# Kernel tuning notes

Hardware: AMD Instinct MI355X
Metric: run time of the kernel (lower is better)

The kernel has to match this reference:

```python
import jax, jax.numpy as jnp
import numpy as np

EPS = 1e-8
M_MARGIN = 0.5  # circle-loss margin m


def _l2norm(x):
    # torch.cosine_similarity clamps the norm product at eps; clamping each norm is equivalent in effect for randn data
    return x / jnp.maximum(jnp.linalg.norm(x, axis=-1, keepdims=True), EPS)


def setup_inputs() -> dict:
    key = jax.random.key(0)
    k1, k2, k3, k4 = jax.random.split(key, 4)
    N, D = 8192, 1024
    return {
        "text_embeddings": jax.random.normal(k1, (N, D), dtype=jnp.float32),
        "text_pos_embeddings": jax.random.normal(k2, (N, D), dtype=jnp.float32),
        "text_neg_embeddings": jax.random.normal(k3, (N, D), dtype=jnp.float32),
        "text_neg_index": jax.random.randint(k4, (N,), 0, N, dtype=jnp.int64 if jax.config.jax_enable_x64 else jnp.int32),
    }


def reference(text_embeddings, text_pos_embeddings, text_neg_embeddings, text_neg_index):
    # use_all_pair=False, mixcse=-1 branch of RetriContrastLoss.forward
    q = _l2norm(text_embeddings)        # [N, D]
    p = _l2norm(text_pos_embeddings)    # [N, D]
    n = _l2norm(text_neg_embeddings)    # [M, D]

    # normalize-then-GEMM == cosine_similarity(unsqueeze(1), unsqueeze(0))
    sim_neg = jnp.einsum("nd,md->nm", q, n)       # [N, M] query-vs-neg cosines
    sim_pos = jnp.sum(q * p, axis=-1)             # [N]    query-vs-pos diagonal cosines
    # NOTE: temperature is never applied in this branch (faithful to source)

    m = M_MARGIN
    # negatives: an = clamp_min(detach(s) + (1+m), 0); s' = an * (s - delta_n), delta_n = -(1-m)
    an = jnp.maximum(jax.lax.stop_gradient(sim_neg) + (1.0 + m), 0.0)
    s_neg = an * (sim_neg + (1.0 - m))
    # positives: ap = clamp_min(-detach(s) + (1+m), 0); s' = -ap * (s - delta_p), delta_p = 1-m
    ap = jnp.maximum(-jax.lax.stop_gradient(sim_pos) + (1.0 + m), 0.0)
    s_pos = -ap * (sim_pos - (1.0 - m))

    # source flattens via boolean mask then logsumexp over dim=0 -> global logsumexp
    lse_neg = jax.scipy.special.logsumexp(s_neg.reshape(-1))
    lse_pos = jax.scipy.special.logsumexp(s_pos)
    return jax.nn.softplus(lse_neg + lse_pos)
```

## Files before the change

### kernel.cpp

```cpp
#include <hip/hip_runtime.h>
#include <hip/hip_bf16.h>
#include <hip/hip_fp8.h>

#define D_K 1024
#define TILE 128
#define ROWB 512
#define KB_ITER 128

typedef int intx8 __attribute__((ext_vector_type(8)));
typedef float floatx4 __attribute__((ext_vector_type(4)));

__device__ __forceinline__ unsigned int f2fp4(float v) {
    const float a = fabsf(v);
    unsigned int c = (unsigned int)(a >= 0.25f) + (a >= 0.75f) + (a >= 1.25f)
                   + (a >= 1.75f) + (a >= 2.5f) + (a >= 3.5f) + (a >= 5.0f);
    return c | (v < 0.0f ? 8u : 0u);
}

__device__ __forceinline__ void gl_lds16(const void* g, void* l) {
    __builtin_amdgcn_global_load_lds(
        (const __attribute__((address_space(1))) unsigned int*)g,
        (__attribute__((address_space(3))) unsigned int*)l,
        16, 0, 0);
}

__device__ __forceinline__ intx8 ld_frag4(const unsigned char* rowbase, int c, int e) {
    const int4 d = *(const int4*)(rowbase + ((c ^ e) * 16));
    intx8 v;
    v[0] = d.x; v[1] = d.y; v[2] = d.z; v[3] = d.w;
    v[4] = 0; v[5] = 0; v[6] = 0; v[7] = 0;
    return v;
}

__global__ __launch_bounds__(256)
void prep_kernel(const float* __restrict__ q, const float* __restrict__ p,
                 const float* __restrict__ ng,
                 unsigned short* __restrict__ qn, unsigned short* __restrict__ nn,
                 float* __restrict__ posp) {
    const int wid = threadIdx.x >> 6, lane = threadIdx.x & 63;
    const int row = blockIdx.x * 4 + wid;
    const size_t base = (size_t)row * D_K;
    const float4* q4 = (const float4*)(q + base);
    const float4* p4 = (const float4*)(p + base);
    const float4* n4 = (const float4*)(ng + base);

    float4 qa[4], na[4];
    float qq = 0.f, pp = 0.f, qp = 0.f, nn2 = 0.f;
#pragma unroll
    for (int j = 0; j < 4; j++) {
        qa[j] = q4[j * 64 + lane];
        float4 pa = p4[j * 64 + lane];
        na[j] = n4[j * 64 + lane];
        qq += qa[j].x*qa[j].x + qa[j].y*qa[j].y + qa[j].z*qa[j].z + qa[j].w*qa[j].w;
        pp += pa.x*pa.x + pa.y*pa.y + pa.z*pa.z + pa.w*pa.w;
        qp += qa[j].x*pa.x + qa[j].y*pa.y + qa[j].z*pa.z + qa[j].w*pa.w;
        nn2 += na[j].x*na[j].x + na[j].y*na[j].y + na[j].z*na[j].z + na[j].w*na[j].w;
    }
#pragma unroll
    for (int off = 1; off < 64; off <<= 1) {
        qq += __shfl_xor(qq, off);
        pp += __shfl_xor(pp, off);
        qp += __shfl_xor(qp, off);
        nn2 += __shfl_xor(nn2, off);
    }
    const float rq = 32.0f / fmaxf(sqrtf(qq), 1e-8f);
    const float rn = 32.0f / fmaxf(sqrtf(nn2), 1e-8f);

    unsigned short* qr = qn + (size_t)row * 256;
    unsigned short* nr = nn + (size_t)row * 256;
#pragma unroll
    for (int j = 0; j < 4; j++) {
        unsigned int w = f2fp4(qa[j].x * rq) | (f2fp4(qa[j].y * rq) << 4)
                       | (f2fp4(qa[j].z * rq) << 8) | (f2fp4(qa[j].w * rq) << 12);
        qr[j * 64 + lane] = (unsigned short)w;
        w = f2fp4(na[j].x * rn) | (f2fp4(na[j].y * rn) << 4)
          | (f2fp4(na[j].z * rn) << 8) | (f2fp4(na[j].w * rn) << 12);
        nr[j * 64 + lane] = (unsigned short)w;
    }

    if (lane == 0) {
        const float rp = 1.0f / fmaxf(sqrtf(pp), 1e-8f);
        const float sim = qp * (rq / 32.0f) * rp;
        const float ap = fmaxf(1.5f - sim, 0.0f);
        const float sp = -ap * (sim - 0.5f);
        posp[row] = __expf(sp - 4.0f);
    }
}

__global__ __launch_bounds__(256, 2)
void gemm_lse_fp4(const unsigned char* __restrict__ A,
                  const unsigned char* __restrict__ B,
                  float* __restrict__ negp) {
    __shared__ unsigned char As[TILE * KB_ITER];
    __shared__ unsigned char Bs[TILE * KB_ITER];

    const int tid = threadIdx.x;
    const int wid = tid >> 6;
    const int lane = tid & 63;
    const int tile_m = blockIdx.y * TILE;
    const int tile_n = blockIdx.x * TILE;

    const int wave_m = (wid & 1) * 64;
    const int wave_n = (wid >> 1) * 64;
    const int quad = lane >> 4;
    const int r = lane & 15;
    const int e = r & 7;

    floatx4 acc[4][4] = {};

    int lds_off[4];
    size_t src_off[4];
#pragma unroll
    for (int s = 0; s < 4; s++) {
        const int cc = s * 256 + tid;
        const int row = cc >> 3, slot = cc & 7;
        lds_off[s] = cc * 16;
        src_off[s] = (size_t)row * ROWB + (size_t)((slot ^ (row & 7)) * 16);
    }
    const unsigned char* Ab = A + (size_t)tile_m * ROWB;
    const unsigned char* Bb = B + (size_t)tile_n * ROWB;

    for (int k0b = 0; k0b < ROWB; k0b += KB_ITER) {
#pragma unroll
        for (int s = 0; s < 4; s++) {
            gl_lds16(Ab + src_off[s] + k0b, &As[lds_off[s]]);
            gl_lds16(Bb + src_off[s] + k0b, &Bs[lds_off[s]]);
        }
        __syncthreads();

#pragma unroll
        for (int t = 0; t < 2; t++) {
            intx8 a[4], b[4];
#pragma unroll
            for (int i = 0; i < 4; i++)
                a[i] = ld_frag4(&As[(wave_m + i * 16 + r) * KB_ITER], t * 4 + quad, e);
#pragma unroll
            for (int j = 0; j < 4; j++)
                b[j] = ld_frag4(&Bs[(wave_n + j * 16 + r) * KB_ITER], t * 4 + quad, e);

#pragma unroll
            for (int i = 0; i < 4; i++)
#pragma unroll
                for (int j = 0; j < 4; j++)
                    acc[i][j] = __builtin_amdgcn_mfma_scale_f32_16x16x128_f8f6f4(
                        a[i], b[j], acc[i][j],
                        4, 4,
                        0, 0x7A7A7A7A,
                        0, 0x7A7A7A7A);
        }

        __syncthreads();
    }

    float lsum = 0.0f;
#pragma unroll
    for (int i = 0; i < 4; i++)
#pragma unroll
        for (int j = 0; j < 4; j++)
#pragma unroll
            for (int el = 0; el < 4; el++) {
                const float s = acc[i][j][el];
                const float an = fmaxf(s + 1.5f, 0.0f);
                const float sn = an * (s + 0.5f);
                lsum += __expf(sn - 4.0f);
            }
    for (int off = 32; off > 0; off >>= 1) lsum += __shfl_down(lsum, off);
    __shared__ float red[4];
    if (lane == 0) red[wid] = lsum;
    __syncthreads();
    if (tid == 0)
        negp[blockIdx.y * gridDim.x + blockIdx.x] = red[0] + red[1] + red[2] + red[3];
}

__global__ __launch_bounds__(1024)
void finalize_kernel(const float* __restrict__ negp, int n_neg,
                     const float* __restrict__ posp, int n_pos,
                     float* __restrict__ out) {
    double sn = 0.0, sp = 0.0;
    for (int i = threadIdx.x; i < n_neg; i += 1024) sn += (double)negp[i];
    for (int i = threadIdx.x; i < n_pos; i += 1024) sp += (double)posp[i];
    for (int off = 32; off > 0; off >>= 1) {
        sn += __shfl_down(sn, off);
        sp += __shfl_down(sp, off);
    }
    __shared__ double rn[16], rp[16];
    const int wid = threadIdx.x >> 6, lane = threadIdx.x & 63;
    if (lane == 0) { rn[wid] = sn; rp[wid] = sp; }
    __syncthreads();
    if (threadIdx.x == 0) {
        double NS = 0.0, PS = 0.0;
#pragma unroll
        for (int w = 0; w < 16; w++) { NS += rn[w]; PS += rp[w]; }
        const double x = (4.0 + log(NS)) + (4.0 + log(PS));
        const double spl = (x > 30.0) ? x : log1p(exp(x));
        out[0] = (float)spl;
    }
}

extern "C" void kernel_launch(void* const* d_in, const int* in_sizes, int n_in,
                              void* d_out, int out_size, void* d_ws, size_t ws_size,
                              hipStream_t stream) {
    const float* q = (const float*)d_in[0];
    const float* p = (const float*)d_in[1];
    const float* ng = (const float*)d_in[2];

    const int N = in_sizes[3];
    const int D = in_sizes[0] / N;
    const int M = in_sizes[2] / D;

    char* ws = (char*)d_ws;
    unsigned short* qn = (unsigned short*)ws;
    unsigned short* nn = (unsigned short*)(ws + (size_t)N * ROWB);
    float* negp = (float*)(ws + (size_t)(N + M) * ROWB);
    const int n_neg = (M / TILE) * (N / TILE);
    float* posp = negp + n_neg;

    prep_kernel<<<N / 4, 256, 0, stream>>>(q, p, ng, qn, nn, posp);
    gemm_lse_fp4<<<dim3(M / TILE, N / TILE), 256, 0, stream>>>(
        (const unsigned char*)qn, (const unsigned char*)nn, negp);
    finalize_kernel<<<1, 1024, 0, stream>>>(negp, n_neg, posp, N, (float*)d_out);
}
```

Measured before the change: 169.5 us.

## Switch FP4 GEMM to 32x32x64 MFMA with larger K stage

Replaces the 16x16x128 scaled MFMA tiling (4x4 fragments per wave) with 32x32x64 scaled MFMAs (2x2 fragments per wave) and doubles the K chunk staged in LDS per iteration to 256 bytes, with a new XOR swizzle. This halves the number of outer loop barriers and fragment loads per MFMA, aiming to reduce LDS traffic and sync overhead. LDS usage doubles (64KB per block), which may limit occupancy to one block per CU despite the launch bound of 2.

New measurement: 174.3 us. 2.9% more time.

```diff
diff --git a/kernel.cpp b/kernel.cpp
--- a/kernel.cpp
+++ b/kernel.cpp
@@ -5,10 +5,10 @@
 #define D_K 1024
 #define TILE 128
 #define ROWB 512
-#define KB_ITER 128
+#define KB_ITER 256
 
 typedef int intx8 __attribute__((ext_vector_type(8)));
-typedef float floatx4 __attribute__((ext_vector_type(4)));
+typedef float floatx16 __attribute__((ext_vector_type(16)));
 
 __device__ __forceinline__ unsigned int f2fp4(float v) {
     const float a = fabsf(v);
@@ -24,12 +24,8 @@
         16, 0, 0);
 }
 
-__device__ __forceinline__ intx8 ld_frag4(const unsigned char* rowbase, int c, int e) {
-    const int4 d = *(const int4*)(rowbase + ((c ^ e) * 16));
-    intx8 v;
-    v[0] = d.x; v[1] = d.y; v[2] = d.z; v[3] = d.w;
-    v[4] = 0; v[5] = 0; v[6] = 0; v[7] = 0;
-    return v;
+__device__ __forceinline__ void ld_lo(intx8* dst, const unsigned char* p) {
+    *(int4*)dst = *(const int4*)p;
 }
 
 __global__ __launch_bounds__(256)
@@ -102,47 +98,49 @@
 
     const int wave_m = (wid & 1) * 64;
     const int wave_n = (wid >> 1) * 64;
-    const int quad = lane >> 4;
-    const int r = lane & 15;
-    const int e = r & 7;
-
-    floatx4 acc[4][4] = {};
-
-    int lds_off[4];
-    size_t src_off[4];
-#pragma unroll
-    for (int s = 0; s < 4; s++) {
-        const int cc = s * 256 + tid;
-        const int row = cc >> 3, slot = cc & 7;
-        lds_off[s] = cc * 16;
-        src_off[s] = (size_t)row * ROWB + (size_t)((slot ^ (row & 7)) * 16);
-    }
+    const int r32 = lane & 31;
+    const int h = lane >> 5;
+    const int e = lane & 7;
+
+    floatx16 acc[2][2] = {};
+
+    intx8 a[2], b[2];
+#pragma unroll
+    for (int i = 0; i < 2; i++) { a[i] = (intx8)0; b[i] = (intx8)0; }
+
     const unsigned char* Ab = A + (size_t)tile_m * ROWB;
     const unsigned char* Bb = B + (size_t)tile_n * ROWB;
 
-    for (int k0b = 0; k0b < ROWB; k0b += KB_ITER) {
-#pragma unroll
-        for (int s = 0; s < 4; s++) {
-            gl_lds16(Ab + src_off[s] + k0b, &As[lds_off[s]]);
-            gl_lds16(Bb + src_off[s] + k0b, &Bs[lds_off[s]]);
+    const unsigned char* arow0 = &As[(wave_m + r32) * KB_ITER];
+    const unsigned char* arow1 = &As[(wave_m + 32 + r32) * KB_ITER];
+    const unsigned char* brow0 = &Bs[(wave_n + r32) * KB_ITER];
+    const unsigned char* brow1 = &Bs[(wave_n + 32 + r32) * KB_ITER];
+
+    for (int kb = 0; kb < ROWB; kb += KB_ITER) {
+#pragma unroll
+        for (int s = 0; s < 8; s++) {
+            const int cc = s * 256 + tid;
+            const int row = cc >> 4, c = cc & 15;
+            const int off = ((c & 8) | ((c & 7) ^ (row & 7))) * 16;
+            gl_lds16(Ab + (size_t)row * ROWB + kb + off, &As[cc * 16]);
+            gl_lds16(Bb + (size_t)row * ROWB + kb + off, &Bs[cc * 16]);
         }
         __syncthreads();
 
 #pragma unroll
-        for (int t = 0; t < 2; t++) {
-            intx8 a[4], b[4];
-#pragma unroll
-            for (int i = 0; i < 4; i++)
-                a[i] = ld_frag4(&As[(wave_m + i * 16 + r) * KB_ITER], t * 4 + quad, e);
-#pragma unroll
-            for (int j = 0; j < 4; j++)
-                b[j] = ld_frag4(&Bs[(wave_n + j * 16 + r) * KB_ITER], t * 4 + quad, e);
-
-#pragma unroll
-            for (int i = 0; i < 4; i++)
-#pragma unroll
-                for (int j = 0; j < 4; j++)
-                    acc[i][j] = __builtin_amdgcn_mfma_scale_f32_16x16x128_f8f6f4(
+        for (int t = 0; t < 8; t++) {
+            const int c = t * 2 + h;
+            const int off = ((c & 8) | ((c & 7) ^ e)) * 16;
+            ld_lo(&a[0], arow0 + off);
+            ld_lo(&a[1], arow1 + off);
+            ld_lo(&b[0], brow0 + off);
+            ld_lo(&b[1], brow1 + off);
+
+#pragma unroll
+            for (int i = 0; i < 2; i++)
+#pragma unroll
+                for (int j = 0; j < 2; j++)
+                    acc[i][j] = __builtin_amdgcn_mfma_scale_f32_32x32x64_f8f6f4(
                         a[i], b[j], acc[i][j],
                         4, 4,
                         0, 0x7A7A7A7A,
@@ -154,11 +152,11 @@
 
     float lsum = 0.0f;
 #pragma unroll
-    for (int i = 0; i < 4; i++)
-#pragma unroll
-        for (int j = 0; j < 4; j++)
-#pragma unroll
-            for (int el = 0; el < 4; el++) {
+    for (int i = 0; i < 2; i++)
+#pragma unroll
+        for (int j = 0; j < 2; j++)
+#pragma unroll
+            for (int el = 0; el < 16; el++) {
                 const float s = acc[i][j][el];
                 const float an = fmaxf(s + 1.5f, 0.0f);
                 const float sn = an * (s + 0.5f);
```
